# Performance work log

Measured on AMD Instinct MI355X. Metric: run time of the kernel, lower is better.

## Reference

```python
import jax, jax.numpy as jnp
import numpy as np

B, N, IDIM, ODIM = 4096, 32, 1024, 1024


def setup_inputs() -> dict:
    key = jax.random.key(0)
    k1, k2, k3 = jax.random.split(key, 3)
    x = jax.random.normal(k1, (B, IDIM), dtype=jnp.float32)
    weight = jax.random.normal(k2, (N, ODIM, IDIM), dtype=jnp.float32)
    gate_w = jax.random.normal(k3, (N, IDIM), dtype=jnp.float32) * (1.0 / np.sqrt(IDIM))
    gate_b = jnp.zeros((N,), dtype=jnp.float32)
    return {"x": x, "weight": weight, "gate_w": gate_w, "gate_b": gate_b}


def reference(x, weight, gate_w, gate_b):
    # per-expert projection: [b, n, odim] (the large intermediate the torch code
    # materializes via einsum 'noi,biz->bnoz' with z=1)
    y = jnp.einsum('noi,bi->bno', weight, x)
    # gate weights: gelu(Linear(idim -> n)) ; torch gelu default is exact (erf)
    g = jax.nn.gelu(x @ gate_w.T + gate_b, approximate=False)  # [b, n]
    # gated combine over experts (the `y @ g` step after rearrange)
    out = jnp.einsum('bno,bn->bo', y, g)  # [b, odim]
    return out
```

## Files before the change

### kernel.cpp

```cpp
#include <hip/hip_runtime.h>
#include <hip/hip_bf16.h>
#include <math.h>


#define BSZ  4096
#define NEXP 32
#define IDIM 1024
#define ODIM 1024

typedef __attribute__((ext_vector_type(8))) short bf16x8;
typedef __attribute__((ext_vector_type(4))) float f32x4;

#define GLOAD_LDS16(g, l) __builtin_amdgcn_global_load_lds( \
    (const __attribute__((address_space(1))) void*)(g),     \
    (__attribute__((address_space(3))) void*)(l), 16, 0, 0)

#define WAITV6 asm volatile("s_waitcnt vmcnt(6)" ::: "memory")
#define WAITV0 asm volatile("s_waitcnt vmcnt(0)" ::: "memory")
#define WAITL0 do { asm volatile("s_waitcnt lgkmcnt(0)" ::: "memory"); \
                    __builtin_amdgcn_sched_barrier(0); } while (0)
#define BARRIER do { __builtin_amdgcn_s_barrier(); \
                     __builtin_amdgcn_sched_barrier(0); } while (0)

__device__ __forceinline__ unsigned short f2bf(float f) {
  unsigned u = __float_as_uint(f);
  unsigned r = (u + 0x7FFFu + ((u >> 16) & 1u)) >> 16;
  return (unsigned short)r;
}

__global__ void zero_kernel(float* __restrict__ out) {
  int i = blockIdx.x * blockDim.x + threadIdx.x;
  ((float4*)out)[i] = make_float4(0.f, 0.f, 0.f, 0.f);
}

__global__ void conv_kernel(const float* __restrict__ in, unsigned short* __restrict__ outb) {
  int i = blockIdx.x * blockDim.x + threadIdx.x;
  const float4* p = (const float4*)in + (size_t)i * 2;
  float4 a = p[0], b = p[1];
  union { bf16x8 v; unsigned short s[8]; } o;
  o.s[0] = f2bf(a.x); o.s[1] = f2bf(a.y); o.s[2] = f2bf(a.z); o.s[3] = f2bf(a.w);
  o.s[4] = f2bf(b.x); o.s[5] = f2bf(b.y); o.s[6] = f2bf(b.z); o.s[7] = f2bf(b.w);
  ((bf16x8*)outb)[i] = o.v;
}

__global__ void gate_kernel(const float* __restrict__ x, const float* __restrict__ gw,
                            const float* __restrict__ gb, float* __restrict__ gT) {
  const int lane = threadIdx.x & 63;
  const int row = blockIdx.x * 4 + (threadIdx.x >> 6);
  const float4* xr = (const float4*)(x + (size_t)row * IDIM);
  float4 xv[4];
#pragma unroll
  for (int t = 0; t < 4; ++t) xv[t] = xr[t * 64 + lane];
  for (int n = 0; n < NEXP; ++n) {
    const float4* wr = (const float4*)(gw + (size_t)n * IDIM);
    float s = 0.f;
#pragma unroll
    for (int t = 0; t < 4; ++t) {
      float4 wv = wr[t * 64 + lane];
      s += xv[t].x * wv.x + xv[t].y * wv.y + xv[t].z * wv.z + xv[t].w * wv.w;
    }
#pragma unroll
    for (int off = 32; off > 0; off >>= 1) s += __shfl_down(s, off, 64);
    if (lane == 0) {
      float v = s + gb[n];
      gT[(size_t)n * BSZ + row] = 0.5f * v * (1.0f + erff(v * 0.70710678118f));
    }
  }
}

__global__ __launch_bounds__(512, 2) void gemm_kernel(
    const unsigned short* __restrict__ xb,
    const unsigned short* __restrict__ wb,
    const float* __restrict__ gT,
    float* __restrict__ out)
{
  __shared__ unsigned short As[3][256 * 64];
  __shared__ unsigned short Bs[3][128 * 64];
  __shared__ float g_lds[16][256];

  const int tid  = threadIdx.x;
  const int lane = tid & 63;
  const int wid  = tid >> 6;
  const int wm   = wid >> 1;
  const int wn   = wid & 1;

  const int orig  = blockIdx.x;
  const int wgid  = (orig & 7) * 32 + (orig >> 3);
  const int mtile = wgid & 15;
  const int grp   = wgid >> 4;
  const int split = grp & 1;
  const int col0  = (grp >> 1) * 128;
  const int row0  = mtile * 256;

  const int srow = lane >> 3;
  const int jsrc = (lane & 7) ^ srow;
  size_t a_off[4], b_off[2];
#pragma unroll
  for (int l = 0; l < 4; ++l)
    a_off[l] = (size_t)(row0 + (wid * 4 + l) * 8 + srow) * IDIM + jsrc * 8;
#pragma unroll
  for (int l = 0; l < 2; ++l)
    b_off[l] = (size_t)(col0 + (wid * 2 + l) * 8 + srow) * IDIM + jsrc * 8;

  const int frow = lane & 15;
  const int hi   = lane >> 4;

  f32x4 acc[4][4], acc_e[4][4];
#pragma unroll
  for (int i = 0; i < 4; ++i)
#pragma unroll
    for (int j = 0; j < 4; ++j) {
      acc[i][j]   = f32x4{0.f, 0.f, 0.f, 0.f};
      acc_e[i][j] = f32x4{0.f, 0.f, 0.f, 0.f};
    }

  {
    const int e = tid >> 5;
    const int r = (tid & 31) * 8;
    const float* src = gT + ((size_t)(split * 16 + e) << 12) + row0 + r;
    *(float4*)&g_lds[e][r]     = *(const float4*)src;
    *(float4*)&g_lds[e][r + 4] = *(const float4*)(src + 4);
  }

  auto STAGE = [&](int buf, int kt) {
    const int e  = kt >> 4;
    const int i0 = (kt & 15) << 6;
    const unsigned short* wb_n = wb + ((size_t)(split * 16 + e) << 20);
#pragma unroll
    for (int l = 0; l < 4; ++l)
      GLOAD_LDS16(xb + a_off[l] + i0, &As[buf][(wid * 4 + l) * 512]);
#pragma unroll
    for (int l = 0; l < 2; ++l)
      GLOAD_LDS16(wb_n + b_off[l] + i0, &Bs[buf][(wid * 2 + l) * 512]);
  };

  __syncthreads();
  STAGE(0, 0);
  STAGE(1, 1);

  int cur = 0;
#pragma unroll 1
  for (int kt = 0; kt < 256; ++kt) {
    if (kt == 255) { WAITV0; } else { WAITV6; }
    BARRIER;
    if (kt < 254) { int s = cur + 2; if (s >= 3) s -= 3; STAGE(s, kt + 2); }

    const unsigned short* A_ = &As[cur][0];
    const unsigned short* B_ = &Bs[cur][0];

    bf16x8 bfr[4][2], afA[2][2];
#pragma unroll
    for (int ni = 0; ni < 4; ++ni)
#pragma unroll
      for (int kk = 0; kk < 2; ++kk) {
        const int r = wn * 64 + ni * 16 + frow;
        const int g = ((kk << 2) + hi) ^ (frow & 7);
        bfr[ni][kk] = *(const bf16x8*)&B_[r * 64 + g * 8];
      }
#pragma unroll
    for (int mi = 0; mi < 2; ++mi)
#pragma unroll
      for (int kk = 0; kk < 2; ++kk) {
        const int r = wm * 64 + mi * 16 + frow;
        const int g = ((kk << 2) + hi) ^ (frow & 7);
        afA[mi][kk] = *(const bf16x8*)&A_[r * 64 + g * 8];
      }
    WAITL0;
    __builtin_amdgcn_s_setprio(1);
#pragma unroll
    for (int mi = 0; mi < 2; ++mi)
#pragma unroll
      for (int ni = 0; ni < 4; ++ni)
#pragma unroll
        for (int kk = 0; kk < 2; ++kk)
          acc_e[mi][ni] = __builtin_amdgcn_mfma_f32_16x16x32_bf16(
              afA[mi][kk], bfr[ni][kk], acc_e[mi][ni], 0, 0, 0);
    __builtin_amdgcn_s_setprio(0);

    bf16x8 afB[2][2];
#pragma unroll
    for (int mi = 0; mi < 2; ++mi)
#pragma unroll
      for (int kk = 0; kk < 2; ++kk) {
        const int r = wm * 64 + (mi + 2) * 16 + frow;
        const int g = ((kk << 2) + hi) ^ (frow & 7);
        afB[mi][kk] = *(const bf16x8*)&A_[r * 64 + g * 8];
      }
    WAITL0;
    __builtin_amdgcn_s_setprio(1);
#pragma unroll
    for (int mi = 0; mi < 2; ++mi)
#pragma unroll
      for (int ni = 0; ni < 4; ++ni)
#pragma unroll
        for (int kk = 0; kk < 2; ++kk)
          acc_e[mi + 2][ni] = __builtin_amdgcn_mfma_f32_16x16x32_bf16(
              afB[mi][kk], bfr[ni][kk], acc_e[mi + 2][ni], 0, 0, 0);
    __builtin_amdgcn_s_setprio(0);

    if ((kt & 15) == 15) {
      const int e = kt >> 4;
#pragma unroll
      for (int mi = 0; mi < 4; ++mi) {
        float4 gv = *(const float4*)&g_lds[e][wm * 64 + mi * 16 + hi * 4];
        f32x4 g4 = f32x4{gv.x, gv.y, gv.z, gv.w};
#pragma unroll
        for (int ni = 0; ni < 4; ++ni) {
          acc[mi][ni] += g4 * acc_e[mi][ni];
          acc_e[mi][ni] = f32x4{0.f, 0.f, 0.f, 0.f};
        }
      }
    }
    if (++cur == 3) cur = 0;
  }

  const int orow0 = row0 + wm * 64 + hi * 4;
  const int ocol0 = col0 + wn * 64 + frow;
#pragma unroll
  for (int mi = 0; mi < 4; ++mi)
#pragma unroll
    for (int j = 0; j < 4; ++j) {
      const int r = orow0 + mi * 16 + j;
#pragma unroll
      for (int ni = 0; ni < 4; ++ni)
        atomicAdd(out + (size_t)r * ODIM + ocol0 + ni * 16, acc[mi][ni][j]);
    }
}

extern "C" void kernel_launch(void* const* d_in, const int* in_sizes, int n_in,
                              void* d_out, int out_size, void* d_ws, size_t ws_size,
                              hipStream_t stream) {
  const float* x  = (const float*)d_in[0];
  const float* w  = (const float*)d_in[1];
  const float* gw = (const float*)d_in[2];
  const float* gb = (const float*)d_in[3];
  float* out = (float*)d_out;

  unsigned short* xb   = (unsigned short*)d_ws;
  unsigned short* wbuf = (unsigned short*)((char*)d_ws + (8u << 20));
  float*          gT   = (float*)((char*)d_ws + (72u << 20));

  zero_kernel<<<(BSZ * ODIM / 4) / 256, 256, 0, stream>>>(out);
  conv_kernel<<<(BSZ * IDIM / 8) / 256, 256, 0, stream>>>(x, xb);
  conv_kernel<<<(NEXP * ODIM * IDIM / 8) / 256, 256, 0, stream>>>(w, wbuf);
  gate_kernel<<<BSZ / 4, 256, 0, stream>>>(x, gw, gb, gT);

  gemm_kernel<<<256, 512, 0, stream>>>(xb, wbuf, gT, out);
}
```

Baseline: 419.7 us.

## Split K-tile into two phases with interleaved half-stage prefetch and barriers

Restructures the main GEMM loop into two k-halves per tile. Each half loads all A and B fragments for one 32-wide k slice, then issues half of the next-next stage's global-to-LDS loads before running 16 MFMAs. Extra workgroup barriers are added so the two phases of all waves stay in lockstep, in the style of a ping-pong schedule. The aim is to spread memory issue across the iteration and overlap it with MFMA work, at the cost of more barriers per iteration.

```diff
diff --git a/kernel.cpp b/kernel.cpp
--- a/kernel.cpp
+++ b/kernel.cpp
@@ -15,12 +15,11 @@
     (const __attribute__((address_space(1))) void*)(g),     \
     (__attribute__((address_space(3))) void*)(l), 16, 0, 0)
 
-#define WAITV6 asm volatile("s_waitcnt vmcnt(6)" ::: "memory")
-#define WAITV0 asm volatile("s_waitcnt vmcnt(0)" ::: "memory")
-#define WAITL0 do { asm volatile("s_waitcnt lgkmcnt(0)" ::: "memory"); \
-                    __builtin_amdgcn_sched_barrier(0); } while (0)
-#define BARRIER do { __builtin_amdgcn_s_barrier(); \
-                     __builtin_amdgcn_sched_barrier(0); } while (0)
+#define SBAR __builtin_amdgcn_sched_barrier(0)
+#define WAITV6 do { asm volatile("s_waitcnt vmcnt(6)" ::: "memory"); SBAR; } while (0)
+#define WAITV0 do { asm volatile("s_waitcnt vmcnt(0)" ::: "memory"); SBAR; } while (0)
+#define WAITL0 do { asm volatile("s_waitcnt lgkmcnt(0)" ::: "memory"); SBAR; } while (0)
+#define BARRIER do { __builtin_amdgcn_s_barrier(); SBAR; } while (0)
 
 __device__ __forceinline__ unsigned short f2bf(float f) {
   unsigned u = __float_as_uint(f);
@@ -122,80 +121,69 @@
     *(float4*)&g_lds[e][r + 4] = *(const float4*)(src + 4);
   }
 
-  auto STAGE = [&](int buf, int kt) {
+  auto STAGE_H = [&](int buf, int kt, int half) {
     const int e  = kt >> 4;
     const int i0 = (kt & 15) << 6;
     const unsigned short* wb_n = wb + ((size_t)(split * 16 + e) << 20);
 #pragma unroll
-    for (int l = 0; l < 4; ++l)
+    for (int l = half * 2; l < half * 2 + 2; ++l)
       GLOAD_LDS16(xb + a_off[l] + i0, &As[buf][(wid * 4 + l) * 512]);
-#pragma unroll
-    for (int l = 0; l < 2; ++l)
-      GLOAD_LDS16(wb_n + b_off[l] + i0, &Bs[buf][(wid * 2 + l) * 512]);
+    GLOAD_LDS16(wb_n + b_off[half] + i0, &Bs[buf][(wid * 2 + half) * 512]);
   };
 
   __syncthreads();
-  STAGE(0, 0);
-  STAGE(1, 1);
+  STAGE_H(0, 0, 0); STAGE_H(0, 0, 1);
+  STAGE_H(1, 1, 0); STAGE_H(1, 1, 1);
+  WAITV6;
+  BARRIER;
 
   int cur = 0;
 #pragma unroll 1
   for (int kt = 0; kt < 256; ++kt) {
-    if (kt == 255) { WAITV0; } else { WAITV6; }
-    BARRIER;
-    if (kt < 254) { int s = cur + 2; if (s >= 3) s -= 3; STAGE(s, kt + 2); }
-
+    int sbuf = cur + 2; if (sbuf >= 3) sbuf -= 3;
     const unsigned short* A_ = &As[cur][0];
     const unsigned short* B_ = &Bs[cur][0];
-
-    bf16x8 bfr[4][2], afA[2][2];
+    const int g0 = hi ^ (frow & 7);
+    const int g1 = (4 + hi) ^ (frow & 7);
+
+    bf16x8 af0[4], bf0[4];
 #pragma unroll
     for (int ni = 0; ni < 4; ++ni)
-#pragma unroll
-      for (int kk = 0; kk < 2; ++kk) {
-        const int r = wn * 64 + ni * 16 + frow;
-        const int g = ((kk << 2) + hi) ^ (frow & 7);
-        bfr[ni][kk] = *(const bf16x8*)&B_[r * 64 + g * 8];
-      }
-#pragma unroll
-    for (int mi = 0; mi < 2; ++mi)
-#pragma unroll
-      for (int kk = 0; kk < 2; ++kk) {
-        const int r = wm * 64 + mi * 16 + frow;
-        const int g = ((kk << 2) + hi) ^ (frow & 7);
-        afA[mi][kk] = *(const bf16x8*)&A_[r * 64 + g * 8];
-      }
+      bf0[ni] = *(const bf16x8*)&B_[(wn * 64 + ni * 16 + frow) * 64 + g0 * 8];
+#pragma unroll
+    for (int mi = 0; mi < 4; ++mi)
+      af0[mi] = *(const bf16x8*)&A_[(wm * 64 + mi * 16 + frow) * 64 + g0 * 8];
+    if (kt < 254) STAGE_H(sbuf, kt + 2, 0);
+    BARRIER;
     WAITL0;
     __builtin_amdgcn_s_setprio(1);
 #pragma unroll
-    for (int mi = 0; mi < 2; ++mi)
+    for (int mi = 0; mi < 4; ++mi)
 #pragma unroll
       for (int ni = 0; ni < 4; ++ni)
-#pragma unroll
-        for (int kk = 0; kk < 2; ++kk)
-          acc_e[mi][ni] = __builtin_amdgcn_mfma_f32_16x16x32_bf16(
-              afA[mi][kk], bfr[ni][kk], acc_e[mi][ni], 0, 0, 0);
+        acc_e[mi][ni] = __builtin_amdgcn_mfma_f32_16x16x32_bf16(
+            af0[mi], bf0[ni], acc_e[mi][ni], 0, 0, 0);
     __builtin_amdgcn_s_setprio(0);
-
-    bf16x8 afB[2][2];
-#pragma unroll
-    for (int mi = 0; mi < 2; ++mi)
-#pragma unroll
-      for (int kk = 0; kk < 2; ++kk) {
-        const int r = wm * 64 + (mi + 2) * 16 + frow;
-        const int g = ((kk << 2) + hi) ^ (frow & 7);
-        afB[mi][kk] = *(const bf16x8*)&A_[r * 64 + g * 8];
-      }
+    BARRIER;
+
+    bf16x8 af1[4], bf1[4];
+#pragma unroll
+    for (int ni = 0; ni < 4; ++ni)
+      bf1[ni] = *(const bf16x8*)&B_[(wn * 64 + ni * 16 + frow) * 64 + g1 * 8];
+#pragma unroll
+    for (int mi = 0; mi < 4; ++mi)
+      af1[mi] = *(const bf16x8*)&A_[(wm * 64 + mi * 16 + frow) * 64 + g1 * 8];
+    if (kt < 254) STAGE_H(sbuf, kt + 2, 1);
+    if (kt < 254) { WAITV6; } else if (kt == 254) { WAITV0; }
+    BARRIER;
     WAITL0;
     __builtin_amdgcn_s_setprio(1);
 #pragma unroll
-    for (int mi = 0; mi < 2; ++mi)
+    for (int mi = 0; mi < 4; ++mi)
 #pragma unroll
       for (int ni = 0; ni < 4; ++ni)
-#pragma unroll
-        for (int kk = 0; kk < 2; ++kk)
-          acc_e[mi + 2][ni] = __builtin_amdgcn_mfma_f32_16x16x32_bf16(
-              afB[mi][kk], bfr[ni][kk], acc_e[mi + 2][ni], 0, 0, 0);
+        acc_e[mi][ni] = __builtin_amdgcn_mfma_f32_16x16x32_bf16(
+            af1[mi], bf1[ni], acc_e[mi][ni], 0, 0, 0);
     __builtin_amdgcn_s_setprio(0);
 
     if ((kt & 15) == 15) {
@@ -211,6 +199,7 @@
         }
       }
     }
+    BARRIER;
     if (++cur == 3) cur = 0;
   }
 
```

New measurement: 347.6 us. 17.2% less time.
